# Kernel optimization log

Hardware: AMD Instinct MI355X
Metric: run time of the kernel (lower is better)

The kernel has to match this reference:

```python
import jax, jax.numpy as jnp
import numpy as np

TEMPERATURE = 0.07
THRESHOLD = 0.7
NUM = 21          # config['data_loader']['args']['class_num']
EPS = 1e-12       # F.normalize eps
NEG_BIG = 1e30


def _nearest_down(x, H, W):
    # torch F.interpolate(mode='nearest'): in_idx = floor(out_idx * in/out)
    Hin, Win = x.shape[-2], x.shape[-1]
    ih = (jnp.arange(H) * Hin) // H
    iw = (jnp.arange(W) * Win) // W
    return x[..., ih[:, None], iw[None, :]]


def _l2n(x):
    return x / jnp.maximum(jnp.linalg.norm(x, axis=1, keepdims=True), EPS)


def setup_inputs() -> dict:
    key = jax.random.key(0)
    ks = jax.random.split(key, 6)
    B, C, H, W = 8, 256, 128, 128
    return {
        "labels": jax.random.randint(ks[0], (B, 512, 512), 0, NUM, dtype=jnp.int64)
        if jax.config.jax_enable_x64 else jax.random.randint(ks[0], (B, 512, 512), 0, NUM, dtype=jnp.int32),
        "features_old": jax.random.normal(ks[1], (B, C, H, W), dtype=jnp.float32),
        "features": jax.random.normal(ks[2], (B, C, H, W), dtype=jnp.float32),
        "outputs_old": jax.random.normal(ks[3], (B, 16, 512, 512), dtype=jnp.float32),
        "outputs": jax.random.normal(ks[4], (B, NUM, 512, 512), dtype=jnp.float32),
        "prototypes": jax.random.normal(ks[5], (NUM, C), dtype=jnp.float32),
        "num_class": 21,
        "num_old_class": 16,
        "num_new_class": 5,
        "epoch": 1,
        "train_step": 1,
        "len_epoch": 100,
    }


def reference(labels, features_old, features, outputs_old, outputs, prototypes,
              num_class, num_old_class, num_new_class, epoch, train_step, len_epoch):
    B, C, H, W = features.shape
    f32 = features.dtype

    # pseudo-label construction
    labels_down = _nearest_down(labels, H, W)                      # [B,H,W] int
    bgr_mask = (labels_down == 0).astype(labels_down.dtype)
    oo = jnp.where(outputs_old < THRESHOLD, 0.0, outputs_old)
    old_pred = jnp.argmax(oo, axis=1)                              # [B,512,512]
    old_down = _nearest_down(old_pred, H, W).astype(labels_down.dtype)
    pseudo = old_down * bgr_mask + labels_down                     # [B,H,W]
    lab = pseudo.reshape(-1)                                       # [N]
    mask = (lab >= 0) & (lab < NUM)

    # [N, C] normalized pixel features
    fa = _l2n(features.transpose(0, 2, 3, 1).reshape(-1, C))
    fo = _l2n(features_old.transpose(0, 2, 3, 1).reshape(-1, C))

    # per-class mean (segment reduce) replacing the python loop over unique labels
    seg = jnp.where(mask, lab, NUM)
    w = mask.astype(f32)
    counts = jax.ops.segment_sum(w, seg, num_segments=NUM + 1)[:NUM]          # [K]
    sum_a = jax.ops.segment_sum(fa * w[:, None], seg, num_segments=NUM + 1)[:NUM]
    sum_o = jax.ops.segment_sum(fo * w[:, None], seg, num_segments=NUM + 1)[:NUM]
    present = counts > 0
    denom = jnp.where(present, counts, 1.0)[:, None]
    anc = jnp.where(present[:, None], sum_a / denom, 0.0)          # [K,C] anchor prototypes
    con_prev = jnp.where(present[:, None], sum_o / denom, 0.0)     # [K,C] old prototypes
    contrast = jax.lax.stop_gradient(jnp.concatenate([anc, con_prev], axis=0))  # [2K,C]

    K = NUM
    eye = jnp.eye(K, dtype=f32)
    rowp = present.astype(f32)                                     # [K]
    colp = jnp.concatenate([rowp, rowp])                           # [2K]
    # labels are unique per row, so R = [I | I]; pos = [0 | I]; neg = 1 - R
    pos_mask = jnp.concatenate([jnp.zeros((K, K), f32), eye], axis=1) * rowp[:, None] * colp[None, :]
    neg_mask = (1.0 - jnp.concatenate([eye, eye], axis=1)) * rowp[:, None] * colp[None, :]

    adc = (anc @ contrast.T) / TEMPERATURE                         # [K,2K]
    # NOTE: faithful to source, negatives use UNshifted logits
    neg = jnp.sum(jnp.exp(adc) * neg_mask, axis=1, keepdims=True)  # [K,1]
    logits_max = jnp.max(jnp.where(colp[None, :] > 0, adc, -NEG_BIG), axis=1, keepdims=True)
    shifted = adc - jax.lax.stop_gradient(logits_max)
    pos_contrast = shifted * pos_mask - jnp.log(jnp.exp(shifted) + neg) * pos_mask

    num = pos_mask.sum(axis=1)
    valid = num > 0
    row_loss = -pos_contrast.sum(axis=1) / jnp.where(valid, num, 1.0)
    loss = jnp.sum(jnp.where(valid, row_loss, 0.0)) / jnp.maximum(jnp.sum(valid.astype(f32)), 1.0)
    return loss
```

## Files before the change

### kernel.cpp

```cpp
#include <hip/hip_runtime.h>
#include <math.h>

#define NPIX   131072
#define CCH    256
#define HW     16384
#define BSTR   4194304
#define NUMC   21
#define KC     5376
#define NREP   16

typedef __attribute__((ext_vector_type(8))) short bf16x8;
typedef __attribute__((ext_vector_type(4))) float f32x4;

static __device__ __forceinline__ uint f2bf(float x) {
    uint u = __builtin_bit_cast(uint, x);
    return (u + 0x7FFFu + ((u >> 16) & 1u)) >> 16;
}
static __device__ __forceinline__ uint ohv(int lbl, int cls, uint iv) {
    return (lbl == cls) ? iv : 0u;
}
static __device__ __forceinline__ float rsq_fast(float x) {
#if __has_builtin(__builtin_amdgcn_rsqf)
    return __builtin_amdgcn_rsqf(x);
#else
    return rsqrtf(x);
#endif
}
static __device__ __forceinline__ uint bfpack_trunc(float x, float y) {
    return __builtin_amdgcn_perm(__builtin_bit_cast(uint, y),
                                 __builtin_bit_cast(uint, x), 0x07060302u);
}

__global__ __launch_bounds__(256) void k_labels(const int* __restrict__ labels,
                                                const float* __restrict__ outputs_old,
                                                int* __restrict__ lab,
                                                float* __restrict__ gcnt)
{
    __shared__ float cnt[NUMC];
    if (threadIdx.x < NUMC) cnt[threadIdx.x] = 0.f;
    __syncthreads();

    int p = blockIdx.x * 256 + threadIdx.x;
    int b = p >> 14;
    int rem = p & 16383;
    int h = rem >> 7;
    int w = rem & 127;
    int ld = labels[b * 262144 + (h * 4) * 512 + (w * 4)];
    int out = ld;
    if (ld == 0) {
        const float* oo = outputs_old + (size_t)b * BSTR + (size_t)(h * 4) * 512 + (w * 4);
        float v0 = oo[0];
        float best = (v0 < 0.7f) ? 0.0f : v0;
        int bi = 0;
        #pragma unroll
        for (int c = 1; c < 16; ++c) {
            float v = oo[(size_t)c * 262144];
            v = (v < 0.7f) ? 0.0f : v;
            if (v > best) { best = v; bi = c; }
        }
        out = bi;
    }
    lab[p] = out;
    unsafeAtomicAdd(&cnt[out], 1.0f);
    __syncthreads();
    if (threadIdx.x < NUMC) unsafeAtomicAdd(&gcnt[threadIdx.x], cnt[threadIdx.x]);
}

__global__ __launch_bounds__(256, 3) void k_msum(const float* __restrict__ fa,
                                                 const float* __restrict__ fo,
                                                 const int* __restrict__ lab,
                                                 float* __restrict__ partA,
                                                 float* __restrict__ partO)
{
    __shared__ ushort tile[2][32 * 256];
    __shared__ float4 ssqP4[2][32];
    __shared__ int    labS[256];

    const int t = threadIdx.x;
    const int w = t >> 6, l = t & 63;
    const int isO = blockIdx.x & 1;
    const float* __restrict__ src = isO ? fo : fa;
    float* part = isO ? partO : partA;

    const int pbase = (blockIdx.x >> 1) * 256;
    const int img   = pbase >> 14;
    const int hw0   = pbase & 16383;
    const float* g  = src + (size_t)img * BSTR + hw0;

    labS[t] = lab[pbase + t];

    const int chb = w * 8 + (l >> 3);
    const int pq  = l & 7;

    f32x4 acc[2][4];
    #pragma unroll
    for (int m = 0; m < 2; ++m)
        #pragma unroll
        for (int n = 0; n < 4; ++n)
            acc[m][n] = (f32x4){0.f, 0.f, 0.f, 0.f};

#define ISSUE(buf, ph) do { \
    _Pragma("unroll") \
    for (int i_ = 0; i_ < 8; ++i_) \
        buf[i_] = *(const float4*)(g + (size_t)(chb + 32 * i_) * HW + (ph) * 32 + pq * 4); \
    } while (0)

#define PHASE(buf, ph, par, pf) do { \
     \
    float sx = 0.f, sy = 0.f, sz = 0.f, sw_ = 0.f; \
    _Pragma("unroll") \
    for (int i_ = 0; i_ < 8; ++i_) { \
        sx += buf[i_].x * buf[i_].x;  sy += buf[i_].y * buf[i_].y; \
        sz += buf[i_].z * buf[i_].z;  sw_ += buf[i_].w * buf[i_].w; \
    } \
    _Pragma("unroll") \
    for (int off_ = 8; off_ < 64; off_ <<= 1) { \
        sx += __shfl_xor(sx, off_, 64);  sy += __shfl_xor(sy, off_, 64); \
        sz += __shfl_xor(sz, off_, 64);  sw_ += __shfl_xor(sw_, off_, 64); \
    } \
    if (l < 8) ssqP4[par][w * 8 + l] = make_float4(sx, sy, sz, sw_); \
     \
    _Pragma("unroll") \
    for (int i_ = 0; i_ < 8; ++i_) { \
        uint lo_ = bfpack_trunc(buf[i_].x, buf[i_].y); \
        uint hi_ = bfpack_trunc(buf[i_].z, buf[i_].w); \
        int ch_ = chb + 32 * i_; \
        *(uint2*)&tile[par][(((pq >> 1) * 256 + ch_) << 3) + ((pq & 1) << 2)] = \
            make_uint2(lo_, hi_); \
    } \
    if (pf) ISSUE(buf, (ph) + 2); \
    __syncthreads(); \
     \
    const int qd_ = (l >> 4) * 2; \
    float4 a0_ = ssqP4[par][qd_],      a1_ = ssqP4[par][8 + qd_]; \
    float4 a2_ = ssqP4[par][16 + qd_], a3_ = ssqP4[par][24 + qd_]; \
    float4 b0_ = ssqP4[par][qd_ + 1],  b1_ = ssqP4[par][9 + qd_]; \
    float4 b2_ = ssqP4[par][17 + qd_], b3_ = ssqP4[par][25 + qd_]; \
    uint iv0 = f2bf(rsq_fast(fmaxf(a0_.x + a1_.x + a2_.x + a3_.x, 1e-24f))); \
    uint iv1 = f2bf(rsq_fast(fmaxf(a0_.y + a1_.y + a2_.y + a3_.y, 1e-24f))); \
    uint iv2 = f2bf(rsq_fast(fmaxf(a0_.z + a1_.z + a2_.z + a3_.z, 1e-24f))); \
    uint iv3 = f2bf(rsq_fast(fmaxf(a0_.w + a1_.w + a2_.w + a3_.w, 1e-24f))); \
    uint iv4 = f2bf(rsq_fast(fmaxf(b0_.x + b1_.x + b2_.x + b3_.x, 1e-24f))); \
    uint iv5 = f2bf(rsq_fast(fmaxf(b0_.y + b1_.y + b2_.y + b3_.y, 1e-24f))); \
    uint iv6 = f2bf(rsq_fast(fmaxf(b0_.z + b1_.z + b2_.z + b3_.z, 1e-24f))); \
    uint iv7 = f2bf(rsq_fast(fmaxf(b0_.w + b1_.w + b2_.w + b3_.w, 1e-24f))); \
     \
    int4 la_ = *(const int4*)&labS[(ph) * 32 + (l >> 4) * 8]; \
    int4 lb_ = *(const int4*)&labS[(ph) * 32 + (l >> 4) * 8 + 4]; \
    const int cls0_ = l & 15, cls1_ = 16 + (l & 15); \
    uint4 u0_, u1_; \
    u0_.x = ohv(la_.x, cls0_, iv0) | (ohv(la_.y, cls0_, iv1) << 16); \
    u0_.y = ohv(la_.z, cls0_, iv2) | (ohv(la_.w, cls0_, iv3) << 16); \
    u0_.z = ohv(lb_.x, cls0_, iv4) | (ohv(lb_.y, cls0_, iv5) << 16); \
    u0_.w = ohv(lb_.z, cls0_, iv6) | (ohv(lb_.w, cls0_, iv7) << 16); \
    u1_.x = ohv(la_.x, cls1_, iv0) | (ohv(la_.y, cls1_, iv1) << 16); \
    u1_.y = ohv(la_.z, cls1_, iv2) | (ohv(la_.w, cls1_, iv3) << 16); \
    u1_.z = ohv(lb_.x, cls1_, iv4) | (ohv(lb_.y, cls1_, iv5) << 16); \
    u1_.w = ohv(lb_.z, cls1_, iv6) | (ohv(lb_.w, cls1_, iv7) << 16); \
    bf16x8 A0_ = __builtin_bit_cast(bf16x8, u0_); \
    bf16x8 A1_ = __builtin_bit_cast(bf16x8, u1_); \
    _Pragma("unroll") \
    for (int n_ = 0; n_ < 4; ++n_) { \
        const int ct_ = w * 4 + n_; \
        const bf16x8 B_ = *(const bf16x8*)&tile[par][((l >> 4) * 256 + ct_ * 16 + (l & 15)) << 3]; \
        acc[0][n_] = __builtin_amdgcn_mfma_f32_16x16x32_bf16(A0_, B_, acc[0][n_], 0, 0, 0); \
        acc[1][n_] = __builtin_amdgcn_mfma_f32_16x16x32_bf16(A1_, B_, acc[1][n_], 0, 0, 0); \
    } \
    } while (0)

    float4 v0[8], v1[8];
    ISSUE(v0, 0);
    ISSUE(v1, 1);

    PHASE(v0, 0, 0, 1);
    PHASE(v1, 1, 1, 1);
    PHASE(v0, 2, 0, 1);
    PHASE(v1, 3, 1, 1);
    PHASE(v0, 4, 0, 1);
    PHASE(v1, 5, 1, 1);
    PHASE(v0, 6, 0, 0);
    PHASE(v1, 7, 1, 0);

#undef ISSUE
#undef PHASE

    const int rep = (blockIdx.x >> 1) & (NREP - 1);
    #pragma unroll
    for (int m = 0; m < 2; ++m)
        #pragma unroll
        for (int n = 0; n < 4; ++n) {
            const int col = (w * 4 + n) * 16 + (l & 15);
            #pragma unroll
            for (int r = 0; r < 4; ++r) {
                const int row = m * 16 + (l >> 4) * 4 + r;
                if (row < NUMC)
                    unsafeAtomicAdd(&part[rep * KC + row * 256 + col], acc[m][n][r]);
            }
        }
}

__global__ __launch_bounds__(256) void k_final(const float* __restrict__ partA,
                                               const float* __restrict__ partO,
                                               const float* __restrict__ gcnt,
                                               float* __restrict__ out)
{
    __shared__ float anc[NUMC * 260];
    __shared__ float con[NUMC * 260];
    __shared__ float adc[NUMC * 44];
    __shared__ float cntS[NUMC];
    __shared__ float rowloss[NUMC];
    __shared__ float rowvalid[NUMC];

    if (threadIdx.x < NUMC) cntS[threadIdx.x] = gcnt[threadIdx.x];
    __syncthreads();
    for (int i = threadIdx.x; i < KC; i += 256) {
        float sA = 0.f, sO = 0.f;
        #pragma unroll
        for (int r = 0; r < NREP; ++r) { sA += partA[r * KC + i]; sO += partO[r * KC + i]; }
        int k = i >> 8, c = i & 255;
        float cn = cntS[k];
        bool pr = cn > 0.f;
        float d = pr ? cn : 1.f;
        anc[k * 260 + c] = pr ? sA / d : 0.f;
        con[k * 260 + c] = pr ? sO / d : 0.f;
    }
    __syncthreads();
    for (int pair = threadIdx.x; pair < NUMC * 2 * NUMC; pair += 256) {
        int k = pair / (2 * NUMC);
        int j = pair % (2 * NUMC);
        const float* ar = anc + k * 260;
        const float* br = (j < NUMC) ? (anc + j * 260) : (con + (j - NUMC) * 260);
        float s = 0.f;
        for (int c = 0; c < CCH; c += 4) {
            float4 a4 = *(const float4*)(ar + c);
            float4 b4 = *(const float4*)(br + c);
            s += a4.x * b4.x + a4.y * b4.y + a4.z * b4.z + a4.w * b4.w;
        }
        adc[k * 44 + j] = s / 0.07f;
    }
    __syncthreads();
    if (threadIdx.x < NUMC) {
        int k = threadIdx.x;
        bool pr = cntS[k] > 0.f;
        float neg = 0.f;
        float mx = -1e30f;
        for (int j = 0; j < 2 * NUMC; ++j) {
            int cj = (j < NUMC) ? j : (j - NUMC);
            bool cp = cntS[cj] > 0.f;
            float v = adc[k * 44 + j];
            if (cp) {
                if (v > mx) mx = v;
                if (j != k && j != NUMC + k) neg += expf(v);
            }
        }
        float sh = adc[k * 44 + NUMC + k] - mx;
        float rl = -(sh - logf(expf(sh) + neg));
        rowloss[k] = pr ? rl : 0.f;
        rowvalid[k] = pr ? 1.f : 0.f;
    }
    __syncthreads();
    if (threadIdx.x == 0) {
        float s = 0.f, v = 0.f;
        for (int kk = 0; kk < NUMC; ++kk) { s += rowloss[kk]; v += rowvalid[kk]; }
        out[0] = s / fmaxf(v, 1.f);
    }
}

extern "C" void kernel_launch(void* const* d_in, const int* in_sizes, int n_in,
                              void* d_out, int out_size, void* d_ws, size_t ws_size,
                              hipStream_t stream) {
    const int*   labels      = (const int*)  d_in[0];
    const float* feats_old   = (const float*)d_in[1];
    const float* feats       = (const float*)d_in[2];
    const float* outputs_old = (const float*)d_in[3];

    float* ws    = (float*)d_ws;
    int*   lab   = (int*)ws;
    float* partA = ws + 131072;
    float* partO = partA + NREP * KC;
    float* gcnt  = partO + NREP * KC;

    hipMemsetAsync(partA, 0, (size_t)(2 * NREP * KC + NUMC) * sizeof(float), stream);

    k_labels<<<NPIX / 256, 256, 0, stream>>>(labels, outputs_old, lab, gcnt);
    k_msum  <<<1024, 256, 0, stream>>>(feats, feats_old, lab, partA, partO);
    k_final <<<1, 256, 0, stream>>>(partA, partO, gcnt, (float*)d_out);
}
```

Before: 96.95 us.

## Restructure msum into 128-pixel chunks with XOR-swizzled channel-major LDS tile

Replaces the eight 32-pixel phases of the masked feature-sum kernel with two 128-pixel chunks. Each chunk loads all 256 channels into a larger XOR-swizzled bf16 LDS tile, computes the per-pixel inverse norms once into shared memory, then runs four MFMA k-steps. The aim is fewer barriers and shuffle reductions per pixel, plus bank-conflict-free LDS reads. In exchange, LDS use grows to about 64KB and the occupancy hint drops from 3 to 2 blocks per SM, so less load latency can be hidden and prefetch overlaps only within a chunk.

```diff
diff --git a/kernel.cpp b/kernel.cpp
--- a/kernel.cpp
+++ b/kernel.cpp
@@ -66,14 +66,15 @@
     if (threadIdx.x < NUMC) unsafeAtomicAdd(&gcnt[threadIdx.x], cnt[threadIdx.x]);
 }
 
-__global__ __launch_bounds__(256, 3) void k_msum(const float* __restrict__ fa,
+__global__ __launch_bounds__(256, 2) void k_msum(const float* __restrict__ fa,
                                                  const float* __restrict__ fo,
                                                  const int* __restrict__ lab,
                                                  float* __restrict__ partA,
                                                  float* __restrict__ partO)
 {
-    __shared__ ushort tile[2][32 * 256];
-    __shared__ float4 ssqP4[2][32];
+    __shared__ ushort tileB[CCH * 128];
+    __shared__ float  ssqP[4][128];
+    __shared__ float  invnS[128];
     __shared__ int    labS[256];
 
     const int t = threadIdx.x;
@@ -89,9 +90,6 @@
 
     labS[t] = lab[pbase + t];
 
-    const int chb = w * 8 + (l >> 3);
-    const int pq  = l & 7;
-
     f32x4 acc[2][4];
     #pragma unroll
     for (int m = 0; m < 2; ++m)
@@ -99,54 +97,34 @@
         for (int n = 0; n < 4; ++n)
             acc[m][n] = (f32x4){0.f, 0.f, 0.f, 0.f};
 
-#define ISSUE(buf, ph) do { \
+#define LOADB(B, i0) do { \
     _Pragma("unroll") \
     for (int i_ = 0; i_ < 8; ++i_) \
-        buf[i_] = *(const float4*)(g + (size_t)(chb + 32 * i_) * HW + (ph) * 32 + pq * 4); \
-    } while (0)
-
-#define PHASE(buf, ph, par, pf) do { \
-     \
-    float sx = 0.f, sy = 0.f, sz = 0.f, sw_ = 0.f; \
+        B[i_] = *(const float4*)(gc + (size_t)(w * 64 + 2 * ((i0) + i_) + (l >> 5)) * HW \
+                                 + (l & 31) * 4); \
+    } while (0)
+
+#define PROCB(B, i0) do { \
     _Pragma("unroll") \
     for (int i_ = 0; i_ < 8; ++i_) { \
-        sx += buf[i_].x * buf[i_].x;  sy += buf[i_].y * buf[i_].y; \
-        sz += buf[i_].z * buf[i_].z;  sw_ += buf[i_].w * buf[i_].w; \
-    } \
-    _Pragma("unroll") \
-    for (int off_ = 8; off_ < 64; off_ <<= 1) { \
-        sx += __shfl_xor(sx, off_, 64);  sy += __shfl_xor(sy, off_, 64); \
-        sz += __shfl_xor(sz, off_, 64);  sw_ += __shfl_xor(sw_, off_, 64); \
-    } \
-    if (l < 8) ssqP4[par][w * 8 + l] = make_float4(sx, sy, sz, sw_); \
-     \
-    _Pragma("unroll") \
-    for (int i_ = 0; i_ < 8; ++i_) { \
-        uint lo_ = bfpack_trunc(buf[i_].x, buf[i_].y); \
-        uint hi_ = bfpack_trunc(buf[i_].z, buf[i_].w); \
-        int ch_ = chb + 32 * i_; \
-        *(uint2*)&tile[par][(((pq >> 1) * 256 + ch_) << 3) + ((pq & 1) << 2)] = \
+        float4 v_ = B[i_]; \
+        s4.x += v_.x * v_.x;  s4.y += v_.y * v_.y; \
+        s4.z += v_.z * v_.z;  s4.w += v_.w * v_.w; \
+        int ch_ = w * 64 + 2 * ((i0) + i_) + (l >> 5); \
+        uint lo_ = bfpack_trunc(v_.x, v_.y); \
+        uint hi_ = bfpack_trunc(v_.z, v_.w); \
+        *(uint2*)((char*)tileB + ch_ * 256 + ((((l & 31) * 8)) ^ ((ch_ & 7) << 4))) = \
             make_uint2(lo_, hi_); \
     } \
-    if (pf) ISSUE(buf, (ph) + 2); \
-    __syncthreads(); \
-     \
-    const int qd_ = (l >> 4) * 2; \
-    float4 a0_ = ssqP4[par][qd_],      a1_ = ssqP4[par][8 + qd_]; \
-    float4 a2_ = ssqP4[par][16 + qd_], a3_ = ssqP4[par][24 + qd_]; \
-    float4 b0_ = ssqP4[par][qd_ + 1],  b1_ = ssqP4[par][9 + qd_]; \
-    float4 b2_ = ssqP4[par][17 + qd_], b3_ = ssqP4[par][25 + qd_]; \
-    uint iv0 = f2bf(rsq_fast(fmaxf(a0_.x + a1_.x + a2_.x + a3_.x, 1e-24f))); \
-    uint iv1 = f2bf(rsq_fast(fmaxf(a0_.y + a1_.y + a2_.y + a3_.y, 1e-24f))); \
-    uint iv2 = f2bf(rsq_fast(fmaxf(a0_.z + a1_.z + a2_.z + a3_.z, 1e-24f))); \
-    uint iv3 = f2bf(rsq_fast(fmaxf(a0_.w + a1_.w + a2_.w + a3_.w, 1e-24f))); \
-    uint iv4 = f2bf(rsq_fast(fmaxf(b0_.x + b1_.x + b2_.x + b3_.x, 1e-24f))); \
-    uint iv5 = f2bf(rsq_fast(fmaxf(b0_.y + b1_.y + b2_.y + b3_.y, 1e-24f))); \
-    uint iv6 = f2bf(rsq_fast(fmaxf(b0_.z + b1_.z + b2_.z + b3_.z, 1e-24f))); \
-    uint iv7 = f2bf(rsq_fast(fmaxf(b0_.w + b1_.w + b2_.w + b3_.w, 1e-24f))); \
-     \
-    int4 la_ = *(const int4*)&labS[(ph) * 32 + (l >> 4) * 8]; \
-    int4 lb_ = *(const int4*)&labS[(ph) * 32 + (l >> 4) * 8 + 4]; \
+    } while (0)
+
+#define KSTEP(c2, ks) do { \
+    float4 ivA_ = *(const float4*)&invnS[(ks) * 32 + (l >> 4) * 8]; \
+    float4 ivB_ = *(const float4*)&invnS[(ks) * 32 + (l >> 4) * 8 + 4]; \
+    uint iv0 = f2bf(ivA_.x), iv1 = f2bf(ivA_.y), iv2 = f2bf(ivA_.z), iv3 = f2bf(ivA_.w); \
+    uint iv4 = f2bf(ivB_.x), iv5 = f2bf(ivB_.y), iv6 = f2bf(ivB_.z), iv7 = f2bf(ivB_.w); \
+    int4 la_ = *(const int4*)&labS[(c2) * 128 + (ks) * 32 + (l >> 4) * 8]; \
+    int4 lb_ = *(const int4*)&labS[(c2) * 128 + (ks) * 32 + (l >> 4) * 8 + 4]; \
     const int cls0_ = l & 15, cls1_ = 16 + (l & 15); \
     uint4 u0_, u1_; \
     u0_.x = ohv(la_.x, cls0_, iv0) | (ohv(la_.y, cls0_, iv1) << 16); \
@@ -161,28 +139,42 @@
     bf16x8 A1_ = __builtin_bit_cast(bf16x8, u1_); \
     _Pragma("unroll") \
     for (int n_ = 0; n_ < 4; ++n_) { \
-        const int ct_ = w * 4 + n_; \
-        const bf16x8 B_ = *(const bf16x8*)&tile[par][((l >> 4) * 256 + ct_ * 16 + (l & 15)) << 3]; \
+        const int chrow_ = (w * 4 + n_) * 16 + (l & 15); \
+        const bf16x8 B_ = *(const bf16x8*)((const char*)tileB + chrow_ * 256 \
+                            + (((ks) * 64 + (l >> 4) * 16) ^ ((chrow_ & 7) << 4))); \
         acc[0][n_] = __builtin_amdgcn_mfma_f32_16x16x32_bf16(A0_, B_, acc[0][n_], 0, 0, 0); \
         acc[1][n_] = __builtin_amdgcn_mfma_f32_16x16x32_bf16(A1_, B_, acc[1][n_], 0, 0, 0); \
     } \
     } while (0)
 
-    float4 v0[8], v1[8];
-    ISSUE(v0, 0);
-    ISSUE(v1, 1);
-
-    PHASE(v0, 0, 0, 1);
-    PHASE(v1, 1, 1, 1);
-    PHASE(v0, 2, 0, 1);
-    PHASE(v1, 3, 1, 1);
-    PHASE(v0, 4, 0, 1);
-    PHASE(v1, 5, 1, 1);
-    PHASE(v0, 6, 0, 0);
-    PHASE(v1, 7, 1, 0);
-
-#undef ISSUE
-#undef PHASE
+#define CHUNK(c2, LAST) do { \
+    const float* gc = g + (c2) * 128; \
+    float4 s4 = {0.f, 0.f, 0.f, 0.f}; \
+    float4 bufA[8], bufB[8]; \
+    LOADB(bufA, 0);  LOADB(bufB, 8); \
+    PROCB(bufA, 0);  LOADB(bufA, 16); \
+    PROCB(bufB, 8);  LOADB(bufB, 24); \
+    PROCB(bufA, 16); PROCB(bufB, 24); \
+    s4.x += __shfl_xor(s4.x, 32, 64);  s4.y += __shfl_xor(s4.y, 32, 64); \
+    s4.z += __shfl_xor(s4.z, 32, 64);  s4.w += __shfl_xor(s4.w, 32, 64); \
+    if (l < 32) *(float4*)&ssqP[w][l * 4] = s4; \
+    __syncthreads(); \
+    if (t < 128) { \
+        float ss_ = ssqP[0][t] + ssqP[1][t] + ssqP[2][t] + ssqP[3][t]; \
+        invnS[t] = rsq_fast(fmaxf(ss_, 1e-24f)); \
+    } \
+    __syncthreads(); \
+    KSTEP(c2, 0); KSTEP(c2, 1); KSTEP(c2, 2); KSTEP(c2, 3); \
+    if (!(LAST)) __syncthreads(); \
+    } while (0)
+
+    CHUNK(0, 0);
+    CHUNK(1, 1);
+
+#undef LOADB
+#undef PROCB
+#undef KSTEP
+#undef CHUNK
 
     const int rep = (blockIdx.x >> 1) & (NREP - 1);
     #pragma unroll
```

Result: no change. 97.43 us, median of 2 (+0.5%).
